# Kernel optimization log

Hardware: AMD Instinct MI355X
Metric: run time of the kernel (lower is better)

Reference implementation:

```python
import jax, jax.numpy as jnp
import numpy as np

N = 65536      # nodes
D = 1024       # d_model
H = 16         # nhead
HD = D // H    # head_dim = 64
K = 4096       # neighbors with local bias
D_EXTRA = 20   # local_bias feature dim
BIAS_DIM = 40  # rbf(16)+seqsep(4)+extra(20)
RES = 0.5      # res_scale
EPS = 1e-5


def _ln(x, w, b):
    mu = x.mean(-1, keepdims=True)
    var = ((x - mu) ** 2).mean(-1, keepdims=True)
    return (x - mu) * jax.lax.rsqrt(var + EPS) * w + b


def setup_inputs() -> dict:
    key = jax.random.key(0)
    ks = jax.random.split(key, 12)
    s = 0.02
    f32 = jnp.float32
    return {
        "h": jax.random.normal(ks[0], (N, D), f32),
        "rbf_ic": jax.random.uniform(ks[1], (N, 16), f32),
        "seqsep_ic": jax.random.uniform(ks[2], (N, 4), f32),
        "local_bias": jax.random.normal(ks[3], (K, D_EXTRA), f32),
        "norm_c_w": jnp.ones((D,), f32), "norm_c_b": jnp.zeros((D,), f32),
        "norm_all_w": jnp.ones((D,), f32), "norm_all_b": jnp.zeros((D,), f32),
        "Wq": jax.random.normal(ks[4], (D, D), f32) * s,
        "Wk": jax.random.normal(ks[5], (D, D), f32) * s,
        "Wv": jax.random.normal(ks[6], (D, D), f32) * s,
        "Wo": jax.random.normal(ks[7], (D, D), f32) * s,
        "Wbias": jax.random.normal(ks[8], (H, BIAS_DIM), f32) * s,
        "gate_W": jax.random.normal(ks[9], (D, 2 * D), f32) * s,
        "gate_b": jnp.zeros((D,), f32),
        "fuse_W1": jax.random.normal(ks[10], (D, 2 * D), f32) * s,
        "fuse_b1": jnp.zeros((D,), f32),
        "fuse_W2": jax.random.normal(ks[11], (D, D), f32) * s,
        "fuse_b2": jnp.zeros((D,), f32),
        "nbr_idx": jnp.arange(K, dtype=jnp.int32),
        "center_idx": 1000,
    }


def _forward(h, rbf_ic, seqsep_ic, local_bias,
             norm_c_w, norm_c_b, norm_all_w, norm_all_b,
             Wq, Wk, Wv, Wo, Wbias,
             gate_W, gate_b, fuse_W1, fuse_b1, fuse_W2, fuse_b2,
             nbr_idx, center_idx):
    c = center_idx
    # bias features: rbf || seqsep || scatter(local_bias)  -> (N, BIAS_DIM)
    full_bias = jnp.zeros((N, D_EXTRA), h.dtype).at[nbr_idx].set(local_bias)
    bias_feat = jnp.concatenate([rbf_ic, seqsep_ic, full_bias], axis=-1)

    h_c = _ln(h[c:c + 1], norm_c_w, norm_c_b)      # (1, D)
    h_all = _ln(h, norm_all_w, norm_all_b)          # (N, D)

    q = (h_c @ Wq.T).reshape(H, HD)                 # (H, HD)
    k = (h_all @ Wk.T).reshape(N, H, HD)            # (N, H, HD)
    v = (h_all @ Wv.T).reshape(N, H, HD)

    logits = jnp.einsum('hd,nhd->hn', q, k) / np.sqrt(HD)   # (H, N)
    logits = logits + (bias_feat @ Wbias.T).T                # add geo bias per head
    w = jax.nn.softmax(logits, axis=-1)                      # (H, N)

    out_center = jnp.einsum('hn,nhd->hd', w, v).reshape(1, D)
    delta_c = out_center @ Wo.T
    h_c_new = h[c:c + 1] + RES * delta_c            # (1, D)

    g = jnp.broadcast_to(h_c_new, (N, D))
    h_cat = jnp.concatenate([h, g], axis=-1)        # (N, 2D)
    gate = jax.nn.sigmoid(h_cat @ gate_W.T + gate_b)
    fused = jax.nn.silu(h_cat @ fuse_W1.T + fuse_b1) @ fuse_W2.T + fuse_b2
    h_new = h + RES * (gate * fused)
    h_new = h_new.at[c].set(h_c_new[0])
    return h_new


def reference(h, rbf_ic, seqsep_ic, local_bias,
              norm_c_w, norm_c_b, norm_all_w, norm_all_b,
              Wq, Wk, Wv, Wo, Wbias,
              gate_W, gate_b, fuse_W1, fuse_b1, fuse_W2, fuse_b2,
              nbr_idx, center_idx):
    return _forward(h, rbf_ic, seqsep_ic, local_bias,
                    norm_c_w, norm_c_b, norm_all_w, norm_all_b,
                    Wq, Wk, Wv, Wo, Wbias,
                    gate_W, gate_b, fuse_W1, fuse_b1, fuse_W2, fuse_b2,
                    nbr_idx, center_idx)
```

## Files before the change

### kernel.cpp

```cpp
#include <hip/hip_runtime.h>
#include <hip/hip_bf16.h>

#define NN 65536
#define DM 1024
#define NH 16
#define KNB 4096
#define DEX 20
#define EPSV 1e-5f

typedef __attribute__((ext_vector_type(8))) short bf16x8;
typedef __attribute__((ext_vector_type(4))) float f32x4;

__device__ __forceinline__ unsigned short f2bf(float f){
  unsigned u = __builtin_bit_cast(unsigned, f);
  u += 0x7fffu + ((u >> 16) & 1u);
  return (unsigned short)(u >> 16);
}
__device__ __forceinline__ float bf2f(unsigned short s){
  return __builtin_bit_cast(float, ((unsigned)s) << 16);
}
__device__ __forceinline__ float wred(float v){
  #pragma unroll
  for (int s = 32; s; s >>= 1) v += __shfl_down(v, s);
  return v;
}

__device__ __forceinline__ bf16x8 ldsr128(const unsigned short* p){
  bf16x8 r;
  unsigned a = (unsigned)(size_t)(const __attribute__((address_space(3))) void*)p;
  asm volatile("ds_read_b128 %0, %1" : "=v"(r) : "v"(a));
  return r;
}

__global__ void k_scatter(const float* __restrict__ lb, const int* __restrict__ nidx,
                          float* __restrict__ extra){
  int i = blockIdx.x * 256 + threadIdx.x;
  if (i < KNB * DEX){
    int j = i / DEX, col = i - j * DEX;
    extra[(size_t)nidx[j] * DEX + col] = lb[i];
  }
}

__global__ void k_convw(const float* __restrict__ gateW, const float* __restrict__ fuseW1,
                        const float* __restrict__ fuseW2,
                        unsigned short* __restrict__ Wcomb, unsigned short* __restrict__ W2b){
  int i = blockIdx.x * 256 + threadIdx.x;
  if (i < 2048 * 1024){
    int o = i >> 10, d = i & 1023;
    float v = (o < 1024) ? gateW[(size_t)o * 2048 + d] : fuseW1[(size_t)(o - 1024) * 2048 + d];
    Wcomb[i] = f2bf(v);
  } else {
    int j = i - 2048 * 1024;
    W2b[j] = f2bf(fuseW2[j]);
  }
}

__global__ void k_cln(const float* __restrict__ h, const int* __restrict__ cidx,
                      const float* __restrict__ cw, const float* __restrict__ cb,
                      float* __restrict__ hcln){
  int t = threadIdx.x, lane = t & 63, wid = t >> 6;
  int c = *cidx;
  const float4 x = *(const float4*)(h + (size_t)c * DM + t * 4);
  float s  = x.x + x.y + x.z + x.w;
  float ss = x.x * x.x + x.y * x.y + x.z * x.z + x.w * x.w;
  __shared__ float rs[4], rq[4];
  s = wred(s); ss = wred(ss);
  if (lane == 0){ rs[wid] = s; rq[wid] = ss; }
  __syncthreads();
  float mean = (rs[0] + rs[1] + rs[2] + rs[3]) * (1.0f / DM);
  float var  = (rq[0] + rq[1] + rq[2] + rq[3]) * (1.0f / DM) - mean * mean;
  float rstd = rsqrtf(var + EPSV);
  const float4 w = *(const float4*)(cw + t * 4);
  const float4 b = *(const float4*)(cb + t * 4);
  float4 o;
  o.x = (x.x - mean) * rstd * w.x + b.x;
  o.y = (x.y - mean) * rstd * w.y + b.y;
  o.z = (x.z - mean) * rstd * w.z + b.z;
  o.w = (x.w - mean) * rstd * w.w + b.w;
  *(float4*)(hcln + t * 4) = o;
}

__global__ void k_q(const float* __restrict__ hcln, const float* __restrict__ Wq,
                    float* __restrict__ q){
  int lane = threadIdx.x & 63, wid = threadIdx.x >> 6;
  float hv[16];
  #pragma unroll
  for (int j = 0; j < 16; j++) hv[j] = hcln[lane + 64 * j];
  #pragma unroll
  for (int oi = 0; oi < 4; oi++){
    int o = blockIdx.x * 16 + wid * 4 + oi;
    const float* wr = Wq + (size_t)o * DM;
    float a = 0.f;
    #pragma unroll
    for (int j = 0; j < 16; j++) a = fmaf(hv[j], wr[lane + 64 * j], a);
    a = wred(a);
    if (lane == 0) q[o] = a;
  }
}

__global__ void k_qkt(const float* __restrict__ q, const float* __restrict__ Wk,
                      float* __restrict__ qkt){
  int idx = blockIdx.x * 256 + threadIdx.x;
  int hh = idx >> 10, i = idx & 1023;
  float a = 0.f;
  #pragma unroll 8
  for (int d = 0; d < 64; d++) a = fmaf(q[hh * 64 + d], Wk[(size_t)(hh * 64 + d) * DM + i], a);
  qkt[idx] = a * 0.125f;
}

__global__ void k_c12(const float* __restrict__ qkt, const float* __restrict__ aw,
                      const float* __restrict__ ab, float* __restrict__ c12){
  const int hh = blockIdx.x >> 1, which = blockIdx.x & 1, lane = threadIdx.x;
  const float* src = which ? ab : aw;
  float a = 0.f;
  #pragma unroll
  for (int j = 0; j < 16; j++) a = fmaf(src[lane + 64 * j], qkt[hh * DM + lane + 64 * j], a);
  a = wred(a);
  if (lane == 0) c12[which * NH + hh] = a;
}

__global__ void k_qa(const float* __restrict__ qkt, const float* __restrict__ aw,
                     unsigned short* __restrict__ Qa){
  const int i = blockIdx.x * 256 + threadIdx.x;
  Qa[i] = f2bf(qkt[i] * aw[i & (DM - 1)]);
}

__global__ void k_bias(const float* __restrict__ rbf, const float* __restrict__ seqsep,
                       const float* __restrict__ extra, const float* __restrict__ wbias,
                       float* __restrict__ biasT){
  const int i = blockIdx.x * 256 + threadIdx.x;
  const int n = i >> 4, hh = i & 15;
  const float* wb = wbias + hh * 40;
  float bb = 0.f;
  #pragma unroll
  for (int j = 0; j < 16; j++) bb = fmaf(rbf[(size_t)n * 16 + j], wb[j], bb);
  #pragma unroll
  for (int j = 0; j < 4; j++)  bb = fmaf(seqsep[(size_t)n * 4 + j], wb[16 + j], bb);
  #pragma unroll
  for (int j = 0; j < 20; j++) bb = fmaf(extra[(size_t)n * DEX + j], wb[20 + j], bb);
  biasT[i] = bb;
}

__global__ void k_lnpass(const float* __restrict__ h, float* __restrict__ meanb,
                         float* __restrict__ rstdb, unsigned short* __restrict__ hbf){
  const int lane = threadIdx.x & 63, w = threadIdx.x >> 6;
  const int gw = blockIdx.x * 4 + w;
  #pragma unroll
  for (int rr = 0; rr < 2; rr++){
    const int n = gw * 2 + rr;
    const float* hp = h + (size_t)n * DM + lane * 16;
    const float4 x0 = *(const float4*)(hp);
    const float4 x1 = *(const float4*)(hp + 4);
    const float4 x2 = *(const float4*)(hp + 8);
    const float4 x3 = *(const float4*)(hp + 12);
    float s  = (x0.x + x0.y + x0.z + x0.w) + (x1.x + x1.y + x1.z + x1.w)
             + (x2.x + x2.y + x2.z + x2.w) + (x3.x + x3.y + x3.z + x3.w);
    float ss = x0.x*x0.x + x0.y*x0.y + x0.z*x0.z + x0.w*x0.w
             + x1.x*x1.x + x1.y*x1.y + x1.z*x1.z + x1.w*x1.w
             + x2.x*x2.x + x2.y*x2.y + x2.z*x2.z + x2.w*x2.w
             + x3.x*x3.x + x3.y*x3.y + x3.z*x3.z + x3.w*x3.w;
    #pragma unroll
    for (int m = 1; m < 64; m <<= 1){ s += __shfl_xor(s, m); ss += __shfl_xor(ss, m); }
    unsigned short* op = hbf + (size_t)n * DM + lane * 16;
    ushort4 o;
    o.x = f2bf(x0.x); o.y = f2bf(x0.y); o.z = f2bf(x0.z); o.w = f2bf(x0.w);
    *(ushort4*)(op) = o;
    o.x = f2bf(x1.x); o.y = f2bf(x1.y); o.z = f2bf(x1.z); o.w = f2bf(x1.w);
    *(ushort4*)(op + 4) = o;
    o.x = f2bf(x2.x); o.y = f2bf(x2.y); o.z = f2bf(x2.z); o.w = f2bf(x2.w);
    *(ushort4*)(op + 8) = o;
    o.x = f2bf(x3.x); o.y = f2bf(x3.y); o.z = f2bf(x3.z); o.w = f2bf(x3.w);
    *(ushort4*)(op + 12) = o;
    if (lane == 0){
      const float mean = s * (1.0f / DM);
      meanb[n] = mean;
      rstdb[n] = rsqrtf(ss * (1.0f / DM) - mean * mean + EPSV);
    }
  }
}

#define MFMA16(a, b, c) __builtin_amdgcn_mfma_f32_16x16x32_bf16(a, b, c, 0, 0, 0)

__launch_bounds__(256)
__global__ void k_logits(const unsigned short* __restrict__ hbf, const unsigned short* __restrict__ Qa,
                         const float* __restrict__ meanb, const float* __restrict__ rstdb,
                         const float* __restrict__ c12, const float* __restrict__ biasT,
                         float* __restrict__ logitsT){
  const int lane = threadIdx.x & 63, w = threadIdx.x >> 6;
  const int n0 = (blockIdx.x * 4 + w) * 16;
  const int fr = lane & 15, kq = lane >> 4;
  f32x4 acc = {0.f, 0.f, 0.f, 0.f};
  const unsigned short* ap = hbf + (size_t)(n0 + fr) * DM + kq * 8;
  const unsigned short* bp = Qa + fr * DM + kq * 8;
  #pragma unroll 4
  for (int kt = 0; kt < DM; kt += 64){
    const bf16x8 a0 = *(const bf16x8*)(ap + kt);
    const bf16x8 b0 = *(const bf16x8*)(bp + kt);
    const bf16x8 a1 = *(const bf16x8*)(ap + kt + 32);
    const bf16x8 b1 = *(const bf16x8*)(bp + kt + 32);
    acc = MFMA16(a0, b0, acc);
    acc = MFMA16(a1, b1, acc);
  }
  const float C1 = c12[fr], C2 = c12[NH + fr];
  #pragma unroll
  for (int r = 0; r < 4; r++){
    const int n = n0 + kq * 4 + r;
    const float mean = meanb[n], rstd = rstdb[n];
    logitsT[(size_t)n * NH + fr] = rstd * acc[r] - rstd * mean * C1 + C2
                                   + biasT[(size_t)n * NH + fr];
  }
}

__global__ void k_smpart(const float* __restrict__ logitsT, float* __restrict__ msp){
  const int t = threadIdx.x, lane = t & 63, w = t >> 6;
  const int hh = lane & 15, no = lane >> 4;
  const float* base = logitsT + ((size_t)blockIdx.x * 256 + w * 64) * NH;
  float m = -3.0e38f;
  #pragma unroll
  for (int it = 0; it < 16; it++)
    m = fmaxf(m, base[(it * 4 + no) * NH + hh]);
  m = fmaxf(m, __shfl_xor(m, 16));
  m = fmaxf(m, __shfl_xor(m, 32));
  float s = 0.f;
  #pragma unroll
  for (int it = 0; it < 16; it++)
    s += __expf(base[(it * 4 + no) * NH + hh] - m);
  s += __shfl_xor(s, 16);
  s += __shfl_xor(s, 32);
  __shared__ float sm[4][16], ssm[4][16];
  if (lane < 16){ sm[w][hh] = m; ssm[w][hh] = s; }
  __syncthreads();
  if (t < NH){
    const float M = fmaxf(fmaxf(sm[0][t], sm[1][t]), fmaxf(sm[2][t], sm[3][t]));
    const float S = ssm[0][t] * __expf(sm[0][t] - M) + ssm[1][t] * __expf(sm[1][t] - M)
                  + ssm[2][t] * __expf(sm[2][t] - M) + ssm[3][t] * __expf(sm[3][t] - M);
    msp[((size_t)blockIdx.x * NH + t) * 2]     = M;
    msp[((size_t)blockIdx.x * NH + t) * 2 + 1] = S;
  }
}

__global__ void k_smcomb(const float* __restrict__ msp, float* __restrict__ ms){
  const int lane = threadIdx.x;
  const int hh = lane & 15, g = lane >> 4;
  float M = -3.0e38f;
  for (int i = g; i < 256; i += 4) M = fmaxf(M, msp[((size_t)i * NH + hh) * 2]);
  M = fmaxf(M, __shfl_xor(M, 16));
  M = fmaxf(M, __shfl_xor(M, 32));
  float S = 0.f;
  for (int i = g; i < 256; i += 4)
    S += msp[((size_t)i * NH + hh) * 2 + 1] * __expf(msp[((size_t)i * NH + hh) * 2] - M);
  S += __shfl_xor(S, 16);
  S += __shfl_xor(S, 32);
  if (lane < NH){ ms[hh] = M; ms[16 + hh] = S; }
}

__global__ void k_expw(const float* __restrict__ logitsT, const float* __restrict__ ms,
                       float* __restrict__ wexp){
  const int i = blockIdx.x * 256 + threadIdx.x;
  const float4 v = ((const float4*)logitsT)[i];
  const int hb = (i & 3) * 4;
  float4 o;
  o.x = __expf(v.x - ms[hb]);
  o.y = __expf(v.y - ms[hb + 1]);
  o.z = __expf(v.z - ms[hb + 2]);
  o.w = __expf(v.w - ms[hb + 3]);
  ((float4*)wexp)[i] = o;
}

#define UB 256
__global__ void k_upart(const unsigned short* __restrict__ hbf, const float* __restrict__ meanb,
                        const float* __restrict__ rstdb, const float* __restrict__ aw,
                        const float* __restrict__ ab, const float* __restrict__ wexp,
                        float* __restrict__ upart){
  const int t = threadIdx.x, bb = blockIdx.x;
  const float4 w  = *(const float4*)(aw + t * 4);
  const float4 bv = *(const float4*)(ab + t * 4);
  float acc[NH][4];
  #pragma unroll
  for (int hh = 0; hh < NH; hh++){ acc[hh][0] = 0.f; acc[hh][1] = 0.f; acc[hh][2] = 0.f; acc[hh][3] = 0.f; }
  #pragma unroll 2
  for (int r = 0; r < NN / UB; r++){
    const int n = bb * (NN / UB) + r;
    const float mean = meanb[n], rstd = rstdb[n];
    const ushort4 hb = *(const ushort4*)(hbf + (size_t)n * DM + t * 4);
    const float l0 = (bf2f(hb.x) - mean) * rstd * w.x + bv.x;
    const float l1 = (bf2f(hb.y) - mean) * rstd * w.y + bv.y;
    const float l2 = (bf2f(hb.z) - mean) * rstd * w.z + bv.z;
    const float l3 = (bf2f(hb.w) - mean) * rstd * w.w + bv.w;
    const float4 e0 = *(const float4*)(wexp + (size_t)n * NH);
    const float4 e1 = *(const float4*)(wexp + (size_t)n * NH + 4);
    const float4 e2 = *(const float4*)(wexp + (size_t)n * NH + 8);
    const float4 e3 = *(const float4*)(wexp + (size_t)n * NH + 12);
#define ACC1(h, e) { acc[h][0] = fmaf(e, l0, acc[h][0]); acc[h][1] = fmaf(e, l1, acc[h][1]); \
                     acc[h][2] = fmaf(e, l2, acc[h][2]); acc[h][3] = fmaf(e, l3, acc[h][3]); }
    ACC1(0, e0.x)  ACC1(1, e0.y)  ACC1(2, e0.z)  ACC1(3, e0.w)
    ACC1(4, e1.x)  ACC1(5, e1.y)  ACC1(6, e1.z)  ACC1(7, e1.w)
    ACC1(8, e2.x)  ACC1(9, e2.y)  ACC1(10, e2.z) ACC1(11, e2.w)
    ACC1(12, e3.x) ACC1(13, e3.y) ACC1(14, e3.z) ACC1(15, e3.w)
#undef ACC1
  }
  #pragma unroll
  for (int hh = 0; hh < NH; hh++){
    float4 o; o.x = acc[hh][0]; o.y = acc[hh][1]; o.z = acc[hh][2]; o.w = acc[hh][3];
    *(float4*)(upart + ((size_t)bb * NH + hh) * DM + t * 4) = o;
  }
}

__global__ void k_ured1(const float* __restrict__ upart, float* __restrict__ up2){
  const int idx = (blockIdx.x & 63) * 256 + threadIdx.x;
  const int sl  = blockIdx.x >> 6;
  float s = 0.f;
  for (int b = sl * 16; b < sl * 16 + 16; b++) s += upart[(size_t)b * (NH * DM) + idx];
  up2[(size_t)sl * (NH * DM) + idx] = s;
}

__global__ void k_ured2(const float* __restrict__ up2, const float* __restrict__ ms,
                        float* __restrict__ u){
  const int idx = blockIdx.x * 256 + threadIdx.x;
  const int hh = idx >> 10;
  float s = 0.f;
  #pragma unroll
  for (int sl = 0; sl < 16; sl++) s += up2[(size_t)sl * (NH * DM) + idx];
  u[idx] = s / ms[16 + hh];
}

__global__ void k_oc(const float* __restrict__ u, const float* __restrict__ Wv,
                     float* __restrict__ oc){
  int lane = threadIdx.x & 63, wid = threadIdx.x >> 6;
  #pragma unroll
  for (int oi = 0; oi < 4; oi++){
    int o = blockIdx.x * 16 + wid * 4 + oi;
    const float* ur = u + (size_t)(o >> 6) * DM;
    const float* wr = Wv + (size_t)o * DM;
    float a = 0.f;
    #pragma unroll
    for (int j = 0; j < 16; j++) a = fmaf(ur[lane + 64 * j], wr[lane + 64 * j], a);
    a = wred(a);
    if (lane == 0) oc[o] = a;
  }
}

__global__ void k_delta(const float* __restrict__ oc, const float* __restrict__ Wo,
                        const float* __restrict__ h, const int* __restrict__ cidx,
                        float* __restrict__ hcnew){
  int lane = threadIdx.x & 63, wid = threadIdx.x >> 6;
  int c = *cidx;
  float ov[16];
  #pragma unroll
  for (int j = 0; j < 16; j++) ov[j] = oc[lane + 64 * j];
  #pragma unroll
  for (int oi = 0; oi < 4; oi++){
    int o = blockIdx.x * 16 + wid * 4 + oi;
    const float* wr = Wo + (size_t)o * DM;
    float a = 0.f;
    #pragma unroll
    for (int j = 0; j < 16; j++) a = fmaf(ov[j], wr[lane + 64 * j], a);
    a = wred(a);
    if (lane == 0) hcnew[o] = h[(size_t)c * DM + o] + 0.5f * a;
  }
}

__global__ void k_gbfb(const float* __restrict__ hcnew, const float* __restrict__ gateW,
                       const float* __restrict__ gateB, const float* __restrict__ fuseW1,
                       const float* __restrict__ fuseB1, float* __restrict__ gbtot,
                       float* __restrict__ fbtot){
  int lane = threadIdx.x & 63, wid = threadIdx.x >> 6;
  float hv[16];
  #pragma unroll
  for (int j = 0; j < 16; j++) hv[j] = hcnew[lane + 64 * j];
  #pragma unroll
  for (int oi = 0; oi < 4; oi++){
    int o = blockIdx.x * 16 + wid * 4 + oi;
    const float* gr = gateW + (size_t)o * 2048 + 1024;
    const float* fr = fuseW1 + (size_t)o * 2048 + 1024;
    float ga = 0.f, fa = 0.f;
    #pragma unroll
    for (int j = 0; j < 16; j++){
      ga = fmaf(hv[j], gr[lane + 64 * j], ga);
      fa = fmaf(hv[j], fr[lane + 64 * j], fa);
    }
    ga = wred(ga); fa = wred(fa);
    if (lane == 0){ gbtot[o] = ga + gateB[o]; fbtot[o] = fa + fuseB1[o]; }
  }
}

#define BM 256
#define BK 64
#define H128 ((size_t)128 * DM)
#define GLL16(gp, lp) __builtin_amdgcn_global_load_lds((const __attribute__((address_space(1))) void*)(gp), (__attribute__((address_space(3))) void*)(lp), 16, 0, 0)
#define SBAR() do { __builtin_amdgcn_sched_barrier(0); \
                    asm volatile("s_barrier" ::: "memory"); \
                    __builtin_amdgcn_sched_barrier(0); } while (0)

#define PHASE(BUF, Q, STG, STL, STK, DOVM) do {                                        \
    if ((Q) == 0){                                                                     \
      _Pragma("unroll")                                                                \
      for (int nj = 0; nj < 4; nj++){                                                  \
        bq[nj][0] = ldsr128(lB + (BUF)*16384 + bBase + nj*1024 + kOff0);               \
        bq[nj][1] = ldsr128(lB + (BUF)*16384 + bBase + nj*1024 + kOff1);               \
      }                                                                                \
    }                                                                                  \
    bf16x8 a00 = ldsr128(lA + (BUF)*16384 + aBase + (2*(Q))*1024   + kOff0);           \
    bf16x8 a01 = ldsr128(lA + (BUF)*16384 + aBase + (2*(Q))*1024   + kOff1);           \
    bf16x8 a10 = ldsr128(lA + (BUF)*16384 + aBase + (2*(Q)+1)*1024 + kOff0);           \
    bf16x8 a11 = ldsr128(lA + (BUF)*16384 + aBase + (2*(Q)+1)*1024 + kOff1);           \
    stage(STG, STL, STK);                                                              \
    SBAR();                                                                            \
    asm volatile("s_waitcnt lgkmcnt(0)" ::: "memory");                                 \
    __builtin_amdgcn_sched_barrier(0);                                                 \
    __builtin_amdgcn_s_setprio(1);                                                     \
    _Pragma("unroll")                                                                  \
    for (int nj = 0; nj < 4; nj++){                                                    \
      acc[2*(Q)][nj]   = MFMA16(a00, bq[nj][0], acc[2*(Q)][nj]);                       \
      acc[2*(Q)][nj]   = MFMA16(a01, bq[nj][1], acc[2*(Q)][nj]);                       \
      acc[2*(Q)+1][nj] = MFMA16(a10, bq[nj][0], acc[2*(Q)+1][nj]);                     \
      acc[2*(Q)+1][nj] = MFMA16(a11, bq[nj][1], acc[2*(Q)+1][nj]);                     \
    }                                                                                  \
    __builtin_amdgcn_s_setprio(0);                                                     \
    if (DOVM){ asm volatile("s_waitcnt vmcnt(4)" ::: "memory"); }                      \
    SBAR();                                                                            \
  } while (0)

template<int MODE>
__launch_bounds__(512, 2)
__global__ void k_gemm(const unsigned short* __restrict__ A, const unsigned short* __restrict__ B,
                       const float* __restrict__ bias0, const float* __restrict__ bias1,
                       const float* __restrict__ hsrc, const unsigned short* __restrict__ gate,
                       unsigned short* __restrict__ og, unsigned short* __restrict__ ot,
                       float* __restrict__ of){
  __shared__ __attribute__((aligned(16))) unsigned short lA[32768];
  __shared__ __attribute__((aligned(16))) unsigned short lB[32768];
  const int NWG = (MODE == 0) ? 2048 : 1024;
  const int NYT = (MODE == 0) ? 8 : 4;
  const int bid = blockIdx.x;
  const int remap = (bid & 7) * (NWG >> 3) + (bid >> 3);
  const int m0 = (remap / NYT) * BM, n0 = (remap % NYT) * BM;

  const int tid = threadIdx.x, lane = tid & 63, w = tid >> 6;
  const int wm = w >> 2, wn = w & 3;

  f32x4 acc[8][4];
  #pragma unroll
  for (int i = 0; i < 8; i++){
    #pragma unroll
    for (int j = 0; j < 4; j++){ acc[i][j][0] = 0.f; acc[i][j][1] = 0.f; acc[i][j][2] = 0.f; acc[i][j][3] = 0.f; }
  }

  const int ln3 = lane >> 3;
  const size_t stRow0 = (size_t)(w * 16 + ln3);
  const int sxor = ((lane & 7) ^ ln3) * 8;
  const size_t srcOff0 = stRow0 * DM + sxor;
  const size_t srcOff1 = (stRow0 + 8) * DM + sxor;
  const int dst0 = w * 1024 + lane * 8;
  const int dst1 = dst0 + 512;

  const unsigned short* gA = A + (size_t)m0 * DM;
  const unsigned short* gB = B + (size_t)n0 * DM;

  auto stage = [&](const unsigned short* g, unsigned short* ldsr, int kt){
    GLL16(g + srcOff0 + kt * 64, ldsr + dst0);
    GLL16(g + srcOff1 + kt * 64, ldsr + dst1);
  };

  const int fr = lane & 15;
  const int kq = lane >> 4;
  const int kOff0 = ((kq)     ^ (lane & 7)) * 8;
  const int kOff1 = ((4 + kq) ^ (lane & 7)) * 8;
  const int aBase = wm * 8192 + fr * 64;
  const int bBase = (wn >> 1) * 8192 + ((wn & 1) * 64 + fr) * 64;

  bf16x8 bq[4][2];

  stage(gA,        lA,                0);
  stage(gA + H128, lA + 8192,         0);
  stage(gB,        lB,                0);
  stage(gB + H128, lB + 8192,         0);
  stage(gB,        lB + 16384,        1);
  stage(gB + H128, lB + 16384 + 8192, 1);
  asm volatile("s_waitcnt vmcnt(4)" ::: "memory");
  SBAR();

  #pragma unroll 1
  for (int i = 0; i < 8; i++){
    const int k0 = 2 * i;
    PHASE(0, 0, gA,        lA + 16384,        k0 + 1,        false);
    PHASE(0, 1, gA + H128, lA + 16384 + 8192, k0 + 1,        false);
    PHASE(0, 2, gB,        lB,                (k0 + 2) & 15, false);
    PHASE(0, 3, gB + H128, lB + 8192,         (k0 + 2) & 15, true);
    PHASE(1, 0, gA,        lA,                (k0 + 2) & 15, false);
    PHASE(1, 1, gA + H128, lA + 8192,         (k0 + 2) & 15, false);
    PHASE(1, 2, gB,        lB + 16384,        (k0 + 3) & 15, false);
    PHASE(1, 3, gB + H128, lB + 16384 + 8192, (k0 + 3) & 15, true);
  }

  const int r0 = kq * 4;
  #pragma unroll
  for (int mi = 0; mi < 8; mi++){
    #pragma unroll
    for (int nj = 0; nj < 4; nj++){
      const int gmb = m0 + wm * 128 + mi * 16 + r0;
      const int gn  = n0 + wn * 64 + nj * 16 + fr;
      #pragma unroll
      for (int r = 0; r < 4; r++){
        const int gm = gmb + r;
        const float x = acc[mi][nj][r];
        if (MODE == 0){
          if (gn < 1024){
            const float v = x + bias0[gn];
            og[(size_t)gm * DM + gn] = f2bf(1.0f / (1.0f + __expf(-v)));
          } else {
            const float v = x + bias1[gn - 1024];
            ot[(size_t)gm * DM + (gn - 1024)] = f2bf(v / (1.0f + __expf(-v)));
          }
        } else {
          const float v = x + bias0[gn];
          const float g = bf2f(gate[(size_t)gm * DM + gn]);
          of[(size_t)gm * DM + gn] = hsrc[(size_t)gm * DM + gn] + 0.5f * g * v;
        }
      }
    }
  }
}

__global__ void k_fixc(const float* __restrict__ hcnew, const int* __restrict__ cidx,
                       float* __restrict__ out){
  int t = threadIdx.x;
  int c = *cidx;
  out[(size_t)c * DM + t] = hcnew[t];
}

extern "C" void kernel_launch(void* const* d_in, const int* in_sizes, int n_in,
                              void* d_out, int out_size, void* d_ws, size_t ws_size,
                              hipStream_t stream){
  const float* h      = (const float*)d_in[0];
  const float* rbf    = (const float*)d_in[1];
  const float* seqsep = (const float*)d_in[2];
  const float* localb = (const float*)d_in[3];
  const float* ncw    = (const float*)d_in[4];
  const float* ncb    = (const float*)d_in[5];
  const float* naw    = (const float*)d_in[6];
  const float* nab    = (const float*)d_in[7];
  const float* Wq     = (const float*)d_in[8];
  const float* Wk     = (const float*)d_in[9];
  const float* Wv     = (const float*)d_in[10];
  const float* Wo     = (const float*)d_in[11];
  const float* Wbias  = (const float*)d_in[12];
  const float* gateW  = (const float*)d_in[13];
  const float* gateB  = (const float*)d_in[14];
  const float* fuseW1 = (const float*)d_in[15];
  const float* fuseB1 = (const float*)d_in[16];
  const float* fuseW2 = (const float*)d_in[17];
  const float* fuseB2 = (const float*)d_in[18];
  const int*   nbr    = (const int*)d_in[19];
  const int*   cidx   = (const int*)d_in[20];
  float* out = (float*)d_out;

  char* p = (char*)d_ws;
  auto alloc = [&](size_t nb){ char* r = p; p += (nb + 255) & ~(size_t)255; return r; };
  float* extra   = (float*)alloc((size_t)NN * DEX * 4);
  float* logitsT = (float*)alloc((size_t)NN * NH * 4);
  float* wexp    = (float*)alloc((size_t)NN * NH * 4);
  float* biasT   = (float*)alloc((size_t)NN * NH * 4);
  float* meanb   = (float*)alloc((size_t)NN * 4);
  float* rstdb   = (float*)alloc((size_t)NN * 4);
  float* ms      = (float*)alloc(32 * 4);
  float* msp     = (float*)alloc((size_t)256 * NH * 2 * 4);
  float* qkt     = (float*)alloc(NH * DM * 4);
  float* u       = (float*)alloc(NH * DM * 4);
  float* hcln    = (float*)alloc(DM * 4);
  float* qv      = (float*)alloc(DM * 4);
  float* oc      = (float*)alloc(DM * 4);
  float* hcnew   = (float*)alloc(DM * 4);
  float* gbtot   = (float*)alloc(DM * 4);
  float* fbtot   = (float*)alloc(DM * 4);
  float* c12     = (float*)alloc(32 * 4);
  float* up2     = (float*)alloc((size_t)16 * NH * DM * 4);
  float* upart   = (float*)alloc((size_t)UB * NH * DM * 4);
  unsigned short* Wcomb = (unsigned short*)alloc((size_t)2048 * 1024 * 2);
  unsigned short* W2b   = (unsigned short*)alloc((size_t)1024 * 1024 * 2);
  unsigned short* Qa    = (unsigned short*)alloc((size_t)NH * DM * 2);
  unsigned short* hbf   = (unsigned short*)alloc((size_t)NN * DM * 2);
  unsigned short* gateb = (unsigned short*)alloc((size_t)NN * DM * 2);
  unsigned short* t1    = (unsigned short*)alloc((size_t)NN * DM * 2);
  if ((size_t)(p - (char*)d_ws) > ws_size) return;

  hipMemsetAsync(extra, 0, (size_t)NN * DEX * 4, stream);
  k_scatter<<<(KNB * DEX + 255) / 256, 256, 0, stream>>>(localb, nbr, extra);
  k_convw<<<(3 * 1024 * 1024) / 256, 256, 0, stream>>>(gateW, fuseW1, fuseW2, Wcomb, W2b);
  k_cln<<<1, 256, 0, stream>>>(h, cidx, ncw, ncb, hcln);
  k_q<<<64, 256, 0, stream>>>(hcln, Wq, qv);
  k_qkt<<<64, 256, 0, stream>>>(qv, Wk, qkt);
  k_c12<<<32, 64, 0, stream>>>(qkt, naw, nab, c12);
  k_qa<<<64, 256, 0, stream>>>(qkt, naw, Qa);
  k_bias<<<NN * NH / 256, 256, 0, stream>>>(rbf, seqsep, extra, Wbias, biasT);
  k_lnpass<<<NN / 8, 256, 0, stream>>>(h, meanb, rstdb, hbf);
  k_logits<<<1024, 256, 0, stream>>>(hbf, Qa, meanb, rstdb, c12, biasT, logitsT);
  k_smpart<<<256, 256, 0, stream>>>(logitsT, msp);
  k_smcomb<<<1, 64, 0, stream>>>(msp, ms);
  k_expw<<<NN * NH / 4 / 256, 256, 0, stream>>>(logitsT, ms, wexp);
  k_upart<<<UB, 256, 0, stream>>>(hbf, meanb, rstdb, naw, nab, wexp, upart);
  k_ured1<<<1024, 256, 0, stream>>>(upart, up2);
  k_ured2<<<64, 256, 0, stream>>>(up2, ms, u);
  k_oc<<<64, 256, 0, stream>>>(u, Wv, oc);
  k_delta<<<64, 256, 0, stream>>>(oc, Wo, h, cidx, hcnew);
  k_gbfb<<<64, 256, 0, stream>>>(hcnew, gateW, gateB, fuseW1, fuseB1, gbtot, fbtot);
  k_gemm<0><<<2048, 512, 0, stream>>>(hbf, Wcomb, gbtot, fbtot, nullptr, nullptr, gateb, t1, nullptr);
  k_gemm<1><<<1024, 512, 0, stream>>>(t1, W2b, fuseB2, nullptr, h, gateb, nullptr, nullptr, out);
  k_fixc<<<1, 1024, 0, stream>>>(hcnew, cidx, out);
}
```

Before: 939.7 us.

## Shrink GEMM tiles to 128x128 with 4 waves and read residual from bf16

Both fused MLP GEMMs move from 256x256 tiles with 8 waves to 128x128 tiles with 4 waves, so the grid has four times as many workgroups. The LDS buffers are halved and the phase schedule is restructured so each phase stages two half-tiles. The second GEMM's epilogue now reads the residual h from the bf16 copy instead of fp32, which halves that read traffic. Smaller tiles lower operand reuse and raise LDS and global traffic per FLOP, and the bf16 residual adds rounding error to the output.

```diff
diff --git a/kernel.cpp b/kernel.cpp
--- a/kernel.cpp
+++ b/kernel.cpp
@@ -384,64 +384,63 @@
   }
 }
 
-#define BM 256
-#define BK 64
-#define H128 ((size_t)128 * DM)
+#define H64 ((size_t)64 * DM)
 #define GLL16(gp, lp) __builtin_amdgcn_global_load_lds((const __attribute__((address_space(1))) void*)(gp), (__attribute__((address_space(3))) void*)(lp), 16, 0, 0)
 #define SBAR() do { __builtin_amdgcn_sched_barrier(0); \
                     asm volatile("s_barrier" ::: "memory"); \
                     __builtin_amdgcn_sched_barrier(0); } while (0)
 
-#define PHASE(BUF, Q, STG, STL, STK, DOVM) do {                                        \
-    if ((Q) == 0){                                                                     \
-      _Pragma("unroll")                                                                \
-      for (int nj = 0; nj < 4; nj++){                                                  \
-        bq[nj][0] = ldsr128(lB + (BUF)*16384 + bBase + nj*1024 + kOff0);               \
-        bq[nj][1] = ldsr128(lB + (BUF)*16384 + bBase + nj*1024 + kOff1);               \
-      }                                                                                \
-    }                                                                                  \
-    bf16x8 a00 = ldsr128(lA + (BUF)*16384 + aBase + (2*(Q))*1024   + kOff0);           \
-    bf16x8 a01 = ldsr128(lA + (BUF)*16384 + aBase + (2*(Q))*1024   + kOff1);           \
-    bf16x8 a10 = ldsr128(lA + (BUF)*16384 + aBase + (2*(Q)+1)*1024 + kOff0);           \
-    bf16x8 a11 = ldsr128(lA + (BUF)*16384 + aBase + (2*(Q)+1)*1024 + kOff1);           \
-    stage(STG, STL, STK);                                                              \
-    SBAR();                                                                            \
-    asm volatile("s_waitcnt lgkmcnt(0)" ::: "memory");                                 \
-    __builtin_amdgcn_sched_barrier(0);                                                 \
-    __builtin_amdgcn_s_setprio(1);                                                     \
-    _Pragma("unroll")                                                                  \
-    for (int nj = 0; nj < 4; nj++){                                                    \
-      acc[2*(Q)][nj]   = MFMA16(a00, bq[nj][0], acc[2*(Q)][nj]);                       \
-      acc[2*(Q)][nj]   = MFMA16(a01, bq[nj][1], acc[2*(Q)][nj]);                       \
-      acc[2*(Q)+1][nj] = MFMA16(a10, bq[nj][0], acc[2*(Q)+1][nj]);                     \
-      acc[2*(Q)+1][nj] = MFMA16(a11, bq[nj][1], acc[2*(Q)+1][nj]);                     \
-    }                                                                                  \
-    __builtin_amdgcn_s_setprio(0);                                                     \
-    if (DOVM){ asm volatile("s_waitcnt vmcnt(4)" ::: "memory"); }                      \
-    SBAR();                                                                            \
+#define PHASE(BUF, QP, STG1, STL1, STG2, STL2, STK, DOVM) do {                         \
+    if ((QP) == 0){                                                                   \
+      _Pragma("unroll")                                                               \
+      for (int nj = 0; nj < 4; nj++){                                                 \
+        bq[nj][0] = ldsr128(lB + (BUF)*8192 + bBase + nj*1024 + kOff0);               \
+        bq[nj][1] = ldsr128(lB + (BUF)*8192 + bBase + nj*1024 + kOff1);               \
+      }                                                                               \
+    }                                                                                 \
+    bf16x8 a00 = ldsr128(lA + (BUF)*8192 + aBase + (2*(QP))*1024   + kOff0);          \
+    bf16x8 a01 = ldsr128(lA + (BUF)*8192 + aBase + (2*(QP))*1024   + kOff1);          \
+    bf16x8 a10 = ldsr128(lA + (BUF)*8192 + aBase + (2*(QP)+1)*1024 + kOff0);          \
+    bf16x8 a11 = ldsr128(lA + (BUF)*8192 + aBase + (2*(QP)+1)*1024 + kOff1);          \
+    stage(STG1, STL1, STK);                                                           \
+    stage(STG2, STL2, STK);                                                           \
+    SBAR();                                                                           \
+    asm volatile("s_waitcnt lgkmcnt(0)" ::: "memory");                                \
+    __builtin_amdgcn_sched_barrier(0);                                                \
+    __builtin_amdgcn_s_setprio(1);                                                    \
+    _Pragma("unroll")                                                                 \
+    for (int nj = 0; nj < 4; nj++){                                                   \
+      acc[2*(QP)][nj]   = MFMA16(a00, bq[nj][0], acc[2*(QP)][nj]);                    \
+      acc[2*(QP)][nj]   = MFMA16(a01, bq[nj][1], acc[2*(QP)][nj]);                    \
+      acc[2*(QP)+1][nj] = MFMA16(a10, bq[nj][0], acc[2*(QP)+1][nj]);                  \
+      acc[2*(QP)+1][nj] = MFMA16(a11, bq[nj][1], acc[2*(QP)+1][nj]);                  \
+    }                                                                                 \
+    __builtin_amdgcn_s_setprio(0);                                                    \
+    if (DOVM){ asm volatile("s_waitcnt vmcnt(4)" ::: "memory"); }                     \
+    SBAR();                                                                           \
   } while (0)
 
 template<int MODE>
-__launch_bounds__(512, 2)
+__launch_bounds__(256, 2)
 __global__ void k_gemm(const unsigned short* __restrict__ A, const unsigned short* __restrict__ B,
                        const float* __restrict__ bias0, const float* __restrict__ bias1,
-                       const float* __restrict__ hsrc, const unsigned short* __restrict__ gate,
+                       const unsigned short* __restrict__ hsrcb, const unsigned short* __restrict__ gate,
                        unsigned short* __restrict__ og, unsigned short* __restrict__ ot,
                        float* __restrict__ of){
-  __shared__ __attribute__((aligned(16))) unsigned short lA[32768];
-  __shared__ __attribute__((aligned(16))) unsigned short lB[32768];
-  const int NWG = (MODE == 0) ? 2048 : 1024;
-  const int NYT = (MODE == 0) ? 8 : 4;
+  __shared__ __attribute__((aligned(16))) unsigned short lA[16384];
+  __shared__ __attribute__((aligned(16))) unsigned short lB[16384];
+  const int NWG = (MODE == 0) ? 8192 : 4096;
+  const int NYT = (MODE == 0) ? 16 : 8;
   const int bid = blockIdx.x;
   const int remap = (bid & 7) * (NWG >> 3) + (bid >> 3);
-  const int m0 = (remap / NYT) * BM, n0 = (remap % NYT) * BM;
+  const int m0 = (remap / NYT) * 128, n0 = (remap % NYT) * 128;
 
   const int tid = threadIdx.x, lane = tid & 63, w = tid >> 6;
-  const int wm = w >> 2, wn = w & 3;
-
-  f32x4 acc[8][4];
-  #pragma unroll
-  for (int i = 0; i < 8; i++){
+  const int wm = w >> 1, wn = w & 1;
+
+  f32x4 acc[4][4];
+  #pragma unroll
+  for (int i = 0; i < 4; i++){
     #pragma unroll
     for (int j = 0; j < 4; j++){ acc[i][j][0] = 0.f; acc[i][j][1] = 0.f; acc[i][j][2] = 0.f; acc[i][j][3] = 0.f; }
   }
@@ -466,39 +465,35 @@
   const int kq = lane >> 4;
   const int kOff0 = ((kq)     ^ (lane & 7)) * 8;
   const int kOff1 = ((4 + kq) ^ (lane & 7)) * 8;
-  const int aBase = wm * 8192 + fr * 64;
-  const int bBase = (wn >> 1) * 8192 + ((wn & 1) * 64 + fr) * 64;
+  const int aBase = wm * 4096 + fr * 64;
+  const int bBase = wn * 4096 + fr * 64;
 
   bf16x8 bq[4][2];
 
-  stage(gA,        lA,                0);
-  stage(gA + H128, lA + 8192,         0);
-  stage(gB,        lB,                0);
-  stage(gB + H128, lB + 8192,         0);
-  stage(gB,        lB + 16384,        1);
-  stage(gB + H128, lB + 16384 + 8192, 1);
+  stage(gA,       lA,        0);
+  stage(gA + H64, lA + 4096, 0);
+  stage(gB,       lB,        0);
+  stage(gB + H64, lB + 4096, 0);
+  stage(gB,       lB + 8192, 1);
+  stage(gB + H64, lB + 8192 + 4096, 1);
   asm volatile("s_waitcnt vmcnt(4)" ::: "memory");
   SBAR();
 
   #pragma unroll 1
   for (int i = 0; i < 8; i++){
     const int k0 = 2 * i;
-    PHASE(0, 0, gA,        lA + 16384,        k0 + 1,        false);
-    PHASE(0, 1, gA + H128, lA + 16384 + 8192, k0 + 1,        false);
-    PHASE(0, 2, gB,        lB,                (k0 + 2) & 15, false);
-    PHASE(0, 3, gB + H128, lB + 8192,         (k0 + 2) & 15, true);
-    PHASE(1, 0, gA,        lA,                (k0 + 2) & 15, false);
-    PHASE(1, 1, gA + H128, lA + 8192,         (k0 + 2) & 15, false);
-    PHASE(1, 2, gB,        lB + 16384,        (k0 + 3) & 15, false);
-    PHASE(1, 3, gB + H128, lB + 16384 + 8192, (k0 + 3) & 15, true);
+    PHASE(0, 0, gA,       lA + 8192, gA + H64, lA + 8192 + 4096, k0 + 1,        false);
+    PHASE(0, 1, gB,       lB,        gB + H64, lB + 4096,        (k0 + 2) & 15, true);
+    PHASE(1, 0, gA,       lA,        gA + H64, lA + 4096,        (k0 + 2) & 15, false);
+    PHASE(1, 1, gB,       lB + 8192, gB + H64, lB + 8192 + 4096, (k0 + 3) & 15, true);
   }
 
   const int r0 = kq * 4;
   #pragma unroll
-  for (int mi = 0; mi < 8; mi++){
+  for (int mi = 0; mi < 4; mi++){
     #pragma unroll
     for (int nj = 0; nj < 4; nj++){
-      const int gmb = m0 + wm * 128 + mi * 16 + r0;
+      const int gmb = m0 + wm * 64 + mi * 16 + r0;
       const int gn  = n0 + wn * 64 + nj * 16 + fr;
       #pragma unroll
       for (int r = 0; r < 4; r++){
@@ -515,7 +510,7 @@
         } else {
           const float v = x + bias0[gn];
           const float g = bf2f(gate[(size_t)gm * DM + gn]);
-          of[(size_t)gm * DM + gn] = hsrc[(size_t)gm * DM + gn] + 0.5f * g * v;
+          of[(size_t)gm * DM + gn] = bf2f(hsrcb[(size_t)gm * DM + gn]) + 0.5f * g * v;
         }
       }
     }
@@ -604,7 +599,7 @@
   k_oc<<<64, 256, 0, stream>>>(u, Wv, oc);
   k_delta<<<64, 256, 0, stream>>>(oc, Wo, h, cidx, hcnew);
   k_gbfb<<<64, 256, 0, stream>>>(hcnew, gateW, gateB, fuseW1, fuseB1, gbtot, fbtot);
-  k_gemm<0><<<2048, 512, 0, stream>>>(hbf, Wcomb, gbtot, fbtot, nullptr, nullptr, gateb, t1, nullptr);
-  k_gemm<1><<<1024, 512, 0, stream>>>(t1, W2b, fuseB2, nullptr, h, gateb, nullptr, nullptr, out);
+  k_gemm<0><<<8192, 256, 0, stream>>>(hbf, Wcomb, gbtot, fbtot, nullptr, nullptr, gateb, t1, nullptr);
+  k_gemm<1><<<4096, 256, 0, stream>>>(t1, W2b, fuseB2, nullptr, hbf, gateb, nullptr, nullptr, out);
   k_fixc<<<1, 1024, 0, stream>>>(hcnew, cidx, out);
 }
```

Measured after the change: 1.006 ms. +7.1%, slower.
